# Kernel tuning notes

Measured on AMD Instinct MI355X. Metric: run time of the kernel, lower is better.

Reference implementation:

```python
import jax, jax.numpy as jnp
import numpy as np


def setup_inputs() -> dict:
    key = jax.random.key(0)
    k_in, k_w, k_b = jax.random.split(key, 3)
    B, S, H, HEADS = 16, 4096, 768, 8
    inputs = jax.random.normal(k_in, (B, S, H), dtype=jnp.float32)
    # xavier_uniform for Linear(H -> HEADS): limit = sqrt(6/(fan_in+fan_out))
    limit = float(np.sqrt(6.0 / (H + HEADS)))
    W = jax.random.uniform(k_w, (HEADS, H), dtype=jnp.float32, minval=-limit, maxval=limit)
    b = jnp.zeros((HEADS,), dtype=jnp.float32)  # nn.Linear default bias init left as zeros-equivalent scale; use uniform per torch default
    bound = float(1.0 / np.sqrt(H))
    b = jax.random.uniform(k_b, (HEADS,), dtype=jnp.float32, minval=-bound, maxval=bound)
    return {"inputs": inputs, "W": W, "b": b}


def reference(inputs, W, b):
    # atten = Linear(inputs) -> [B, S, heads]; transpose -> [B, heads, S]
    atten = jnp.einsum("bsh,eh->bes", inputs, W) + b[None, :, None]  # [B, heads, S]
    atten_sm = jax.nn.softmax(atten, axis=-1)                        # softmax over seq
    out = jnp.einsum("bes,bsh->beh", atten_sm, inputs)               # [B, heads, H]
    return (out, atten)
```

## Files before the change

### kernel.cpp

```cpp
#include <hip/hip_runtime.h>
#include <math.h>

constexpr int Bn = 16;
constexpr int Sn = 4096;
constexpr int Hn = 768;
constexpr int En = 8;
constexpr int OUT_N = Bn * En * Hn;
constexpr int NBLK  = 512;
constexpr int NSC   = 32;
constexpr int SLOTS = 5;
constexpr int WFSZ  = SLOTS * Hn;
constexpr int LSUM  = 4 * WFSZ;

typedef const __attribute__((address_space(1))) void gvoid;
typedef __attribute__((address_space(3))) void svoid;

__global__ __launch_bounds__(256, 2) void k_fused(
    const float* __restrict__ x, const float* __restrict__ W,
    const float* __restrict__ bias, float* __restrict__ att,
    float* __restrict__ part, float* __restrict__ sumexpG) {
  __shared__ float sh[4 * WFSZ + 32];
  const int lane = threadIdx.x & 63;
  const int w    = threadIdx.x >> 6;
  const int wid  = blockIdx.x * 4 + w;
  const int b    = wid >> 7;
  const int wl   = wid & 127;

  float4 wf[8][3];
#pragma unroll
  for (int e = 0; e < 8; ++e)
#pragma unroll
    for (int j = 0; j < 3; ++j)
      wf[e][j] = *(const float4*)(W + e * 768 + (lane << 2) + (j << 8));
  const float bv = bias[lane & 7];

  float4 acc[8][3];
#pragma unroll
  for (int e = 0; e < 8; ++e)
#pragma unroll
    for (int j = 0; j < 3; ++j) acc[e][j] = make_float4(0.f, 0.f, 0.f, 0.f);
  float sume = 0.0f;

  float* fifo = sh + w * WFSZ;
  const float* xr = x + (size_t)(b * Sn + wl) * Hn;

#pragma unroll
  for (int k = 0; k < 4; ++k) {
    const float* rp = xr + (size_t)(k * 128) * Hn;
    float* dst = fifo + k * Hn;
#pragma unroll
    for (int c = 0; c < 3; ++c)
      __builtin_amdgcn_global_load_lds((gvoid*)(rp + (c << 8) + (lane << 2)),
                                       (svoid*)(dst + (c << 8)), 16, 0, 0);
  }

  int sp = 0, pf = 4;
  for (int t = 0; t < 32; ++t) {
    if (t < 30) asm volatile("s_waitcnt vmcnt(9)" ::: "memory");
    else        asm volatile("s_waitcnt vmcnt(0)" ::: "memory");

    const float4* s4 = (const float4*)(fifo + sp * Hn);
    const float4 c0 = s4[lane], c1 = s4[lane + 64], c2 = s4[lane + 128];

    float a8[8];
#pragma unroll
    for (int e = 0; e < 8; ++e) {
      float a = c0.x * wf[e][0].x;
      a = fmaf(c0.y, wf[e][0].y, a);
      a = fmaf(c0.z, wf[e][0].z, a);
      a = fmaf(c0.w, wf[e][0].w, a);
      a = fmaf(c1.x, wf[e][1].x, a);
      a = fmaf(c1.y, wf[e][1].y, a);
      a = fmaf(c1.z, wf[e][1].z, a);
      a = fmaf(c1.w, wf[e][1].w, a);
      a = fmaf(c2.x, wf[e][2].x, a);
      a = fmaf(c2.y, wf[e][2].y, a);
      a = fmaf(c2.z, wf[e][2].z, a);
      a = fmaf(c2.w, wf[e][2].w, a);
      a8[e] = a;
    }

    float v4[4];
#pragma unroll
    for (int k = 0; k < 4; ++k) {
      const float pa = a8[2 * k], pb = a8[2 * k + 1];
      const bool hi = (lane & 1);
      const float send = hi ? pa : pb;
      const float keep = hi ? pb : pa;
      v4[k] = keep + __shfl_xor(send, 1, 64);
    }
    float v2[2];
#pragma unroll
    for (int k = 0; k < 2; ++k) {
      const float pa = v4[2 * k], pb = v4[2 * k + 1];
      const bool hi = (lane & 2);
      const float send = hi ? pa : pb;
      const float keep = hi ? pb : pa;
      v2[k] = keep + __shfl_xor(send, 2, 64);
    }
    float u;
    {
      const float pa = v2[0], pb = v2[1];
      const bool hi = (lane & 4);
      const float send = hi ? pa : pb;
      const float keep = hi ? pb : pa;
      u = keep + __shfl_xor(send, 4, 64);
    }
    u += __shfl_xor(u, 8, 64);
    u += __shfl_xor(u, 16, 64);
    u += __shfl_xor(u, 32, 64);

    const float logit = u + bv;
    const int s = wl + (t << 7);
    if (lane < 8) att[(size_t)((b << 3) + lane) * Sn + s] = logit;

    const float texp = __expf(logit);
    sume += texp;

#pragma unroll
    for (int e = 0; e < 8; ++e) {
      const float we = __shfl(texp, e, 64);
      acc[e][0].x = fmaf(we, c0.x, acc[e][0].x);
      acc[e][0].y = fmaf(we, c0.y, acc[e][0].y);
      acc[e][0].z = fmaf(we, c0.z, acc[e][0].z);
      acc[e][0].w = fmaf(we, c0.w, acc[e][0].w);
      acc[e][1].x = fmaf(we, c1.x, acc[e][1].x);
      acc[e][1].y = fmaf(we, c1.y, acc[e][1].y);
      acc[e][1].z = fmaf(we, c1.z, acc[e][1].z);
      acc[e][1].w = fmaf(we, c1.w, acc[e][1].w);
      acc[e][2].x = fmaf(we, c2.x, acc[e][2].x);
      acc[e][2].y = fmaf(we, c2.y, acc[e][2].y);
      acc[e][2].z = fmaf(we, c2.z, acc[e][2].z);
      acc[e][2].w = fmaf(we, c2.w, acc[e][2].w);
    }

    if (t < 28) {
      const float* rp = xr + (size_t)((t + 4) * 128) * Hn;
      float* dst = fifo + pf * Hn;
#pragma unroll
      for (int c = 0; c < 3; ++c)
        __builtin_amdgcn_global_load_lds((gvoid*)(rp + (c << 8) + (lane << 2)),
                                         (svoid*)(dst + (c << 8)), 16, 0, 0);
    }
    sp = (sp + 1 == SLOTS) ? 0 : sp + 1;
    pf = (pf + 1 == SLOTS) ? 0 : pf + 1;
  }

  if (lane < 8) sh[LSUM + w * 8 + lane] = sume;
#pragma unroll
  for (int half = 0; half < 2; ++half) {
    __syncthreads();
    if (w > 0) {
      float4* dst = (float4*)sh + (size_t)(w - 1) * 768;
#pragma unroll
      for (int e = 0; e < 4; ++e)
#pragma unroll
        for (int j = 0; j < 3; ++j)
          dst[(e * 3 + j) * 64 + lane] = acc[half * 4 + e][j];
    }
    __syncthreads();
    if (w == 0) {
#pragma unroll
      for (int g = 0; g < 3; ++g) {
        const float4* src = (const float4*)sh + (size_t)g * 768;
#pragma unroll
        for (int e = 0; e < 4; ++e)
#pragma unroll
          for (int j = 0; j < 3; ++j) {
            const float4 v = src[(e * 3 + j) * 64 + lane];
            float4& a = acc[half * 4 + e][j];
            a.x += v.x; a.y += v.y; a.z += v.z; a.w += v.w;
          }
      }
    }
  }
  if (w == 0) {
    float4* po = (float4*)(part + (size_t)blockIdx.x * (En * Hn));
#pragma unroll
    for (int e = 0; e < 8; ++e)
#pragma unroll
      for (int j = 0; j < 3; ++j)
        po[e * 192 + j * 64 + lane] = acc[e][j];
    if (lane < 8)
      sumexpG[blockIdx.x * 8 + lane] = sh[LSUM + lane] + sh[LSUM + 8 + lane] +
                                       sh[LSUM + 16 + lane] + sh[LSUM + 24 + lane];
  }
}

__global__ __launch_bounds__(256) void k_final(const float* __restrict__ part,
                                               const float* __restrict__ sumexpG,
                                               float* __restrict__ out) {
  __shared__ float Zs[128];
  const int t = threadIdx.x;
  if (t < 128) {
    const int b = t >> 3, e = t & 7;
    float z = 0.0f;
    for (int c = 0; c < NSC; ++c) z += sumexpG[((b * NSC + c) << 3) + e];
    Zs[t] = 1.0f / z;
  }
  __syncthreads();

  const int o4 = blockIdx.x * 256 + t;
  const int b  = o4 / 1536;
  const int r4 = o4 - b * 1536;
  const int e  = r4 / 192;
  const float4* p4 = (const float4*)part + (size_t)(b * NSC) * 1536 + r4;
  float4 a = make_float4(0.f, 0.f, 0.f, 0.f);
  for (int c = 0; c < NSC; ++c) {
    const float4 v = p4[(size_t)c * 1536];
    a.x += v.x; a.y += v.y; a.z += v.z; a.w += v.w;
  }
  const float inv = Zs[(b << 3) + e];
  a.x *= inv; a.y *= inv; a.z *= inv; a.w *= inv;
  ((float4*)out)[o4] = a;
}

extern "C" void kernel_launch(void* const* d_in, const int* in_sizes, int n_in,
                              void* d_out, int out_size, void* d_ws, size_t ws_size,
                              hipStream_t stream) {
  const float* x    = (const float*)d_in[0];
  const float* W    = (const float*)d_in[1];
  const float* bias = (const float*)d_in[2];
  float* out = (float*)d_out;
  float* att = out + OUT_N;
  float* part    = (float*)d_ws;
  float* sumexpG = part + NBLK * En * Hn;

  k_fused<<<NBLK, 256, 0, stream>>>(x, W, bias, att, part, sumexpG);
  k_final<<<OUT_N / 4 / 256, 256, 0, stream>>>(part, sumexpG, out);
}
```

Before: 287.8 us.

## Fuse final reduction into main kernel via per-batch atomic counters

Removes the separate k_final launch. Each block now signals completion on a per-batch atomic counter, and six blocks per batch spin until all 32 blocks of that batch have finished, then reduce the partials and normalize. The block-level partial reduction is also spread across all four waves instead of funnelling through wave 0. This trades a kernel launch and its tail for spin-waiting, a memset, and a dependence on all blocks being co-resident (512 blocks at 2 per CU is likely fine on this GPU).

```diff
diff --git a/kernel.cpp b/kernel.cpp
--- a/kernel.cpp
+++ b/kernel.cpp
@@ -7,7 +7,6 @@
 constexpr int En = 8;
 constexpr int OUT_N = Bn * En * Hn;
 constexpr int NBLK  = 512;
-constexpr int NSC   = 32;
 constexpr int SLOTS = 5;
 constexpr int WFSZ  = SLOTS * Hn;
 constexpr int LSUM  = 4 * WFSZ;
@@ -18,11 +17,13 @@
 __global__ __launch_bounds__(256, 2) void k_fused(
     const float* __restrict__ x, const float* __restrict__ W,
     const float* __restrict__ bias, float* __restrict__ att,
-    float* __restrict__ part, float* __restrict__ sumexpG) {
+    float* __restrict__ part, float* __restrict__ sumexpG,
+    unsigned* ctr, float* __restrict__ out) {
   __shared__ float sh[4 * WFSZ + 32];
   const int lane = threadIdx.x & 63;
   const int w    = threadIdx.x >> 6;
-  const int wid  = blockIdx.x * 4 + w;
+  const int blk  = blockIdx.x;
+  const int wid  = blk * 4 + w;
   const int b    = wid >> 7;
   const int wl   = wid & 127;
 
@@ -147,72 +148,74 @@
   }
 
   if (lane < 8) sh[LSUM + w * 8 + lane] = sume;
+  float4* eb = (float4*)sh;
+  float* po = part + (size_t)blk * (En * Hn);
 #pragma unroll
   for (int half = 0; half < 2; ++half) {
     __syncthreads();
-    if (w > 0) {
-      float4* dst = (float4*)sh + (size_t)(w - 1) * 768;
-#pragma unroll
-      for (int e = 0; e < 4; ++e)
-#pragma unroll
-        for (int j = 0; j < 3; ++j)
-          dst[(e * 3 + j) * 64 + lane] = acc[half * 4 + e][j];
-    }
-    __syncthreads();
-    if (w == 0) {
-#pragma unroll
-      for (int g = 0; g < 3; ++g) {
-        const float4* src = (const float4*)sh + (size_t)g * 768;
-#pragma unroll
-        for (int e = 0; e < 4; ++e)
-#pragma unroll
-          for (int j = 0; j < 3; ++j) {
-            const float4 v = src[(e * 3 + j) * 64 + lane];
-            float4& a = acc[half * 4 + e][j];
-            a.x += v.x; a.y += v.y; a.z += v.z; a.w += v.w;
-          }
+#pragma unroll
+    for (int e = 0; e < 4; ++e)
+#pragma unroll
+      for (int j = 0; j < 3; ++j)
+        eb[((w * 4 + e) * 3 + j) * 64 + lane] = acc[half * 4 + e][j];
+    __syncthreads();
+    if ((w >> 1) == half) {
+      const int lh = (w & 1) * 2;
+#pragma unroll
+      for (int p = 0; p < 2; ++p) {
+        const int le = lh + p, ge = half * 4 + le;
+#pragma unroll
+        for (int j = 0; j < 3; ++j) {
+          float4 v        = eb[((0 + le) * 3 + j) * 64 + lane];
+          const float4 v1 = eb[((4 + le) * 3 + j) * 64 + lane];
+          const float4 v2 = eb[((8 + le) * 3 + j) * 64 + lane];
+          const float4 v3 = eb[((12 + le) * 3 + j) * 64 + lane];
+          v.x += v1.x; v.y += v1.y; v.z += v1.z; v.w += v1.w;
+          v.x += v2.x; v.y += v2.y; v.z += v2.z; v.w += v2.w;
+          v.x += v3.x; v.y += v3.y; v.z += v3.z; v.w += v3.w;
+          *(float4*)(po + (size_t)ge * Hn + (j << 8) + (lane << 2)) = v;
+        }
       }
     }
   }
-  if (w == 0) {
-    float4* po = (float4*)(part + (size_t)blockIdx.x * (En * Hn));
-#pragma unroll
-    for (int e = 0; e < 8; ++e)
-#pragma unroll
-      for (int j = 0; j < 3; ++j)
-        po[e * 192 + j * 64 + lane] = acc[e][j];
-    if (lane < 8)
-      sumexpG[blockIdx.x * 8 + lane] = sh[LSUM + lane] + sh[LSUM + 8 + lane] +
-                                       sh[LSUM + 16 + lane] + sh[LSUM + 24 + lane];
-  }
-}
-
-__global__ __launch_bounds__(256) void k_final(const float* __restrict__ part,
-                                               const float* __restrict__ sumexpG,
-                                               float* __restrict__ out) {
-  __shared__ float Zs[128];
-  const int t = threadIdx.x;
-  if (t < 128) {
-    const int b = t >> 3, e = t & 7;
-    float z = 0.0f;
-    for (int c = 0; c < NSC; ++c) z += sumexpG[((b * NSC + c) << 3) + e];
-    Zs[t] = 1.0f / z;
-  }
+  if (w == 0 && lane < 8)
+    sumexpG[(blk << 3) + lane] = sh[LSUM + lane] + sh[LSUM + 8 + lane] +
+                                 sh[LSUM + 16 + lane] + sh[LSUM + 24 + lane];
+
   __syncthreads();
-
-  const int o4 = blockIdx.x * 256 + t;
-  const int b  = o4 / 1536;
-  const int r4 = o4 - b * 1536;
-  const int e  = r4 / 192;
-  const float4* p4 = (const float4*)part + (size_t)(b * NSC) * 1536 + r4;
-  float4 a = make_float4(0.f, 0.f, 0.f, 0.f);
-  for (int c = 0; c < NSC; ++c) {
-    const float4 v = p4[(size_t)c * 1536];
-    a.x += v.x; a.y += v.y; a.z += v.z; a.w += v.w;
-  }
-  const float inv = Zs[(b << 3) + e];
-  a.x *= inv; a.y *= inv; a.z *= inv; a.w *= inv;
-  ((float4*)out)[o4] = a;
+  if (threadIdx.x == 0) {
+    __threadfence();
+    __hip_atomic_fetch_add(ctr + b, 1u, __ATOMIC_RELEASE,
+                           __HIP_MEMORY_SCOPE_AGENT);
+  }
+
+  const int c6 = blk & 31;
+  if (c6 < 6) {
+    if (threadIdx.x == 0) {
+      while (__hip_atomic_load(ctr + b, __ATOMIC_ACQUIRE,
+                               __HIP_MEMORY_SCOPE_AGENT) < 32u)
+        __builtin_amdgcn_s_sleep(8);
+    }
+    __syncthreads();
+    if (threadIdx.x < 8) {
+      float z = 0.0f;
+      for (int cc = 0; cc < 32; ++cc)
+        z += sumexpG[(((b << 5) + cc) << 3) + threadIdx.x];
+      sh[threadIdx.x] = 1.0f / z;
+    }
+    __syncthreads();
+    const int r4 = (c6 << 8) + threadIdx.x;
+    const int e  = r4 / 192;
+    const float4* p4 = (const float4*)part + (size_t)(b << 5) * 1536 + r4;
+    float4 a = make_float4(0.f, 0.f, 0.f, 0.f);
+    for (int cc = 0; cc < 32; ++cc) {
+      const float4 v = p4[(size_t)cc * 1536];
+      a.x += v.x; a.y += v.y; a.z += v.z; a.w += v.w;
+    }
+    const float inv = sh[e];
+    a.x *= inv; a.y *= inv; a.z *= inv; a.w *= inv;
+    ((float4*)out)[(size_t)b * 1536 + r4] = a;
+  }
 }
 
 extern "C" void kernel_launch(void* const* d_in, const int* in_sizes, int n_in,
@@ -225,7 +228,8 @@
   float* att = out + OUT_N;
   float* part    = (float*)d_ws;
   float* sumexpG = part + NBLK * En * Hn;
-
-  k_fused<<<NBLK, 256, 0, stream>>>(x, W, bias, att, part, sumexpG);
-  k_final<<<OUT_N / 4 / 256, 256, 0, stream>>>(part, sumexpG, out);
+  unsigned* ctr  = (unsigned*)(sumexpG + NBLK * En);
+
+  hipMemsetAsync(ctr, 0, Bn * sizeof(unsigned), stream);
+  k_fused<<<NBLK, 256, 0, stream>>>(x, W, bias, att, part, sumexpG, ctr, out);
 }
```

New measurement: 318.4 us. +10.6%, slower.

## Split heads across wave pairs sharing a two-row LDS FIFO

Applied to the files above, without the earlier changes.

Each pair of waves now shares one LDS FIFO holding two sequence rows per slot, and each wave handles only 4 of the 8 heads for both rows. This halves the per-wave weight and accumulator register footprint. It also simplifies the end-of-block reduction to a single LDS exchange between wave pairs. The cost is a __syncthreads in every loop iteration so the two waves can see each other's async loads, plus somewhat more shuffle work per row.

```diff
diff --git a/kernel.cpp b/kernel.cpp
--- a/kernel.cpp
+++ b/kernel.cpp
@@ -9,45 +9,64 @@
 constexpr int NBLK  = 512;
 constexpr int NSC   = 32;
 constexpr int SLOTS = 5;
-constexpr int WFSZ  = SLOTS * Hn;
-constexpr int LSUM  = 4 * WFSZ;
+constexpr int PFIFO = SLOTS * 2 * Hn;
+constexpr int LSUM  = 2 * PFIFO;
 
 typedef const __attribute__((address_space(1))) void gvoid;
 typedef __attribute__((address_space(3))) void svoid;
+
+__device__ __forceinline__ float dot12(const float4 c0, const float4 c1,
+                                       const float4 c2, const float4 w0,
+                                       const float4 w1, const float4 w2) {
+  float a = c0.x * w0.x;
+  a = fmaf(c0.y, w0.y, a); a = fmaf(c0.z, w0.z, a); a = fmaf(c0.w, w0.w, a);
+  a = fmaf(c1.x, w1.x, a); a = fmaf(c1.y, w1.y, a); a = fmaf(c1.z, w1.z, a);
+  a = fmaf(c1.w, w1.w, a);
+  a = fmaf(c2.x, w2.x, a); a = fmaf(c2.y, w2.y, a); a = fmaf(c2.z, w2.z, a);
+  a = fmaf(c2.w, w2.w, a);
+  return a;
+}
+
+__device__ __forceinline__ void fma4(float4& a, const float s, const float4 c) {
+  a.x = fmaf(s, c.x, a.x); a.y = fmaf(s, c.y, a.y);
+  a.z = fmaf(s, c.z, a.z); a.w = fmaf(s, c.w, a.w);
+}
 
 __global__ __launch_bounds__(256, 2) void k_fused(
     const float* __restrict__ x, const float* __restrict__ W,
     const float* __restrict__ bias, float* __restrict__ att,
     float* __restrict__ part, float* __restrict__ sumexpG) {
-  __shared__ float sh[4 * WFSZ + 32];
+  __shared__ float sh[2 * PFIFO + 16];
   const int lane = threadIdx.x & 63;
   const int w    = threadIdx.x >> 6;
-  const int wid  = blockIdx.x * 4 + w;
-  const int b    = wid >> 7;
-  const int wl   = wid & 127;
-
-  float4 wf[8][3];
-#pragma unroll
-  for (int e = 0; e < 8; ++e)
+  const int pr   = w >> 1;
+  const int hw   = w & 1;
+  const int blk  = blockIdx.x;
+  const int b    = blk >> 5;
+  const int ps   = ((blk & 31) << 1) + pr;
+
+  float4 wf[4][3];
+#pragma unroll
+  for (int e = 0; e < 4; ++e)
 #pragma unroll
     for (int j = 0; j < 3; ++j)
-      wf[e][j] = *(const float4*)(W + e * 768 + (lane << 2) + (j << 8));
-  const float bv = bias[lane & 7];
-
-  float4 acc[8][3];
-#pragma unroll
-  for (int e = 0; e < 8; ++e)
+      wf[e][j] = *(const float4*)(W + (hw * 4 + e) * Hn + (j << 8) + (lane << 2));
+  const float bv = bias[hw * 4 + (lane & 3)];
+
+  float4 acc[4][3];
+#pragma unroll
+  for (int e = 0; e < 4; ++e)
 #pragma unroll
     for (int j = 0; j < 3; ++j) acc[e][j] = make_float4(0.f, 0.f, 0.f, 0.f);
   float sume = 0.0f;
 
-  float* fifo = sh + w * WFSZ;
-  const float* xr = x + (size_t)(b * Sn + wl) * Hn;
+  float* fifo = sh + pr * PFIFO;
+  const float* xb = x + (size_t)b * Sn * Hn;
 
 #pragma unroll
   for (int k = 0; k < 4; ++k) {
-    const float* rp = xr + (size_t)(k * 128) * Hn;
-    float* dst = fifo + k * Hn;
+    const float* rp = xb + (size_t)((k << 7) + (hw << 6) + ps) * Hn;
+    float* dst = fifo + k * (2 * Hn) + hw * Hn;
 #pragma unroll
     for (int c = 0; c < 3; ++c)
       __builtin_amdgcn_global_load_lds((gvoid*)(rp + (c << 8) + (lane << 2)),
@@ -56,87 +75,69 @@
 
   int sp = 0, pf = 4;
   for (int t = 0; t < 32; ++t) {
-    if (t < 30) asm volatile("s_waitcnt vmcnt(9)" ::: "memory");
+    if (t < 28) asm volatile("s_waitcnt vmcnt(9)" ::: "memory");
     else        asm volatile("s_waitcnt vmcnt(0)" ::: "memory");
-
-    const float4* s4 = (const float4*)(fifo + sp * Hn);
-    const float4 c0 = s4[lane], c1 = s4[lane + 64], c2 = s4[lane + 128];
-
-    float a8[8];
-#pragma unroll
-    for (int e = 0; e < 8; ++e) {
-      float a = c0.x * wf[e][0].x;
-      a = fmaf(c0.y, wf[e][0].y, a);
-      a = fmaf(c0.z, wf[e][0].z, a);
-      a = fmaf(c0.w, wf[e][0].w, a);
-      a = fmaf(c1.x, wf[e][1].x, a);
-      a = fmaf(c1.y, wf[e][1].y, a);
-      a = fmaf(c1.z, wf[e][1].z, a);
-      a = fmaf(c1.w, wf[e][1].w, a);
-      a = fmaf(c2.x, wf[e][2].x, a);
-      a = fmaf(c2.y, wf[e][2].y, a);
-      a = fmaf(c2.z, wf[e][2].z, a);
-      a = fmaf(c2.w, wf[e][2].w, a);
-      a8[e] = a;
-    }
-
-    float v4[4];
-#pragma unroll
-    for (int k = 0; k < 4; ++k) {
-      const float pa = a8[2 * k], pb = a8[2 * k + 1];
+    __syncthreads();
+
+    const float4* s4 = (const float4*)(fifo + sp * (2 * Hn));
+    const float4 c0 = s4[lane],       c1 = s4[lane + 64],  c2 = s4[lane + 128];
+    const float4 d0 = s4[lane + 192], d1 = s4[lane + 256], d2 = s4[lane + 320];
+
+    float a4[4], g4[4];
+#pragma unroll
+    for (int e = 0; e < 4; ++e) {
+      a4[e] = dot12(c0, c1, c2, wf[e][0], wf[e][1], wf[e][2]);
+      g4[e] = dot12(d0, d1, d2, wf[e][0], wf[e][1], wf[e][2]);
+    }
+
+    float av[2], gv[2];
+#pragma unroll
+    for (int k = 0; k < 2; ++k) {
       const bool hi = (lane & 1);
-      const float send = hi ? pa : pb;
-      const float keep = hi ? pb : pa;
-      v4[k] = keep + __shfl_xor(send, 1, 64);
-    }
-    float v2[2];
-#pragma unroll
-    for (int k = 0; k < 2; ++k) {
-      const float pa = v4[2 * k], pb = v4[2 * k + 1];
+      const float as = hi ? a4[2 * k] : a4[2 * k + 1];
+      const float ak = hi ? a4[2 * k + 1] : a4[2 * k];
+      av[k] = ak + __shfl_xor(as, 1, 64);
+      const float gs = hi ? g4[2 * k] : g4[2 * k + 1];
+      const float gk = hi ? g4[2 * k + 1] : g4[2 * k];
+      gv[k] = gk + __shfl_xor(gs, 1, 64);
+    }
+    float ua, ug;
+    {
       const bool hi = (lane & 2);
-      const float send = hi ? pa : pb;
-      const float keep = hi ? pb : pa;
-      v2[k] = keep + __shfl_xor(send, 2, 64);
-    }
-    float u;
-    {
-      const float pa = v2[0], pb = v2[1];
-      const bool hi = (lane & 4);
-      const float send = hi ? pa : pb;
-      const float keep = hi ? pb : pa;
-      u = keep + __shfl_xor(send, 4, 64);
-    }
-    u += __shfl_xor(u, 8, 64);
-    u += __shfl_xor(u, 16, 64);
-    u += __shfl_xor(u, 32, 64);
-
-    const float logit = u + bv;
-    const int s = wl + (t << 7);
-    if (lane < 8) att[(size_t)((b << 3) + lane) * Sn + s] = logit;
-
-    const float texp = __expf(logit);
-    sume += texp;
-
-#pragma unroll
-    for (int e = 0; e < 8; ++e) {
-      const float we = __shfl(texp, e, 64);
-      acc[e][0].x = fmaf(we, c0.x, acc[e][0].x);
-      acc[e][0].y = fmaf(we, c0.y, acc[e][0].y);
-      acc[e][0].z = fmaf(we, c0.z, acc[e][0].z);
-      acc[e][0].w = fmaf(we, c0.w, acc[e][0].w);
-      acc[e][1].x = fmaf(we, c1.x, acc[e][1].x);
-      acc[e][1].y = fmaf(we, c1.y, acc[e][1].y);
-      acc[e][1].z = fmaf(we, c1.z, acc[e][1].z);
-      acc[e][1].w = fmaf(we, c1.w, acc[e][1].w);
-      acc[e][2].x = fmaf(we, c2.x, acc[e][2].x);
-      acc[e][2].y = fmaf(we, c2.y, acc[e][2].y);
-      acc[e][2].z = fmaf(we, c2.z, acc[e][2].z);
-      acc[e][2].w = fmaf(we, c2.w, acc[e][2].w);
+      const float as = hi ? av[0] : av[1];
+      const float ak = hi ? av[1] : av[0];
+      ua = ak + __shfl_xor(as, 2, 64);
+      const float gs = hi ? gv[0] : gv[1];
+      const float gk = hi ? gv[1] : gv[0];
+      ug = gk + __shfl_xor(gs, 2, 64);
+    }
+    ua += __shfl_xor(ua, 4, 64);  ug += __shfl_xor(ug, 4, 64);
+    ua += __shfl_xor(ua, 8, 64);  ug += __shfl_xor(ug, 8, 64);
+    ua += __shfl_xor(ua, 16, 64); ug += __shfl_xor(ug, 16, 64);
+    ua += __shfl_xor(ua, 32, 64); ug += __shfl_xor(ug, 32, 64);
+
+    const float la = ua + bv, lg = ug + bv;
+    const int s0 = (t << 7) + ps;
+    if (lane < 4) {
+      float* ap = att + (size_t)((b << 3) + (hw << 2) + lane) * Sn + s0;
+      ap[0]  = la;
+      ap[64] = lg;
+    }
+
+    const float ea = __expf(la), eg = __expf(lg);
+    sume += ea + eg;
+
+#pragma unroll
+    for (int e = 0; e < 4; ++e) {
+      const float wa = __shfl(ea, e, 64);
+      const float wg = __shfl(eg, e, 64);
+      fma4(acc[e][0], wa, c0); fma4(acc[e][1], wa, c1); fma4(acc[e][2], wa, c2);
+      fma4(acc[e][0], wg, d0); fma4(acc[e][1], wg, d1); fma4(acc[e][2], wg, d2);
     }
 
     if (t < 28) {
-      const float* rp = xr + (size_t)((t + 4) * 128) * Hn;
-      float* dst = fifo + pf * Hn;
+      const float* rp = xb + (size_t)(((t + 4) << 7) + (hw << 6) + ps) * Hn;
+      float* dst = fifo + pf * (2 * Hn) + hw * Hn;
 #pragma unroll
       for (int c = 0; c < 3; ++c)
         __builtin_amdgcn_global_load_lds((gvoid*)(rp + (c << 8) + (lane << 2)),
@@ -146,44 +147,30 @@
     pf = (pf + 1 == SLOTS) ? 0 : pf + 1;
   }
 
-  if (lane < 8) sh[LSUM + w * 8 + lane] = sume;
-#pragma unroll
-  for (int half = 0; half < 2; ++half) {
-    __syncthreads();
-    if (w > 0) {
-      float4* dst = (float4*)sh + (size_t)(w - 1) * 768;
-#pragma unroll
-      for (int e = 0; e < 4; ++e)
-#pragma unroll
-        for (int j = 0; j < 3; ++j)
-          dst[(e * 3 + j) * 64 + lane] = acc[half * 4 + e][j];
-    }
-    __syncthreads();
-    if (w == 0) {
-#pragma unroll
-      for (int g = 0; g < 3; ++g) {
-        const float4* src = (const float4*)sh + (size_t)g * 768;
-#pragma unroll
-        for (int e = 0; e < 4; ++e)
-#pragma unroll
-          for (int j = 0; j < 3; ++j) {
-            const float4 v = src[(e * 3 + j) * 64 + lane];
-            float4& a = acc[half * 4 + e][j];
-            a.x += v.x; a.y += v.y; a.z += v.z; a.w += v.w;
-          }
+  if (lane < 4) sh[LSUM + w * 4 + lane] = sume;
+  __syncthreads();
+  float4* eb = (float4*)sh;
+  if (w >= 2) {
+#pragma unroll
+    for (int e = 0; e < 4; ++e)
+#pragma unroll
+      for (int j = 0; j < 3; ++j)
+        eb[(((w - 2) * 4 + e) * 3 + j) * 64 + lane] = acc[e][j];
+  }
+  __syncthreads();
+  if (w < 2) {
+    float* po = part + (size_t)blk * (En * Hn) + (size_t)(w * 4) * Hn;
+#pragma unroll
+    for (int e = 0; e < 4; ++e)
+#pragma unroll
+      for (int j = 0; j < 3; ++j) {
+        const float4 v = eb[((w * 4 + e) * 3 + j) * 64 + lane];
+        float4 a = acc[e][j];
+        a.x += v.x; a.y += v.y; a.z += v.z; a.w += v.w;
+        *(float4*)(po + e * Hn + (j << 8) + (lane << 2)) = a;
       }
-    }
-  }
-  if (w == 0) {
-    float4* po = (float4*)(part + (size_t)blockIdx.x * (En * Hn));
-#pragma unroll
-    for (int e = 0; e < 8; ++e)
-#pragma unroll
-      for (int j = 0; j < 3; ++j)
-        po[e * 192 + j * 64 + lane] = acc[e][j];
-    if (lane < 8)
-      sumexpG[blockIdx.x * 8 + lane] = sh[LSUM + lane] + sh[LSUM + 8 + lane] +
-                                       sh[LSUM + 16 + lane] + sh[LSUM + 24 + lane];
+    if (w == 0 && lane < 8)
+      sumexpG[(blk << 3) + lane] = sh[LSUM + lane] + sh[LSUM + 8 + lane];
   }
 }
 
```

Result: no change. 285.9 us (-0.7%).
